# Kernel tuning notes

Hardware: AMD Instinct MI355X
Metric: run time of the kernel (lower is better)

## Reference

```python
import jax, jax.numpy as jnp
import numpy as np

B, N, F, T = 16, 1024, 32, 12
K, FC, FT, TS, D = 3, 64, 64, 1, 16
THETA_THR = 0.6
LN_EPS = 1e-5


def setup_inputs() -> dict:
    key = jax.random.key(0)
    ks = jax.random.split(key, 20)
    r = lambda i, shape, s=0.1: jax.random.normal(ks[i], shape, dtype=jnp.float32) * s
    return dict(
        x=jax.random.normal(ks[0], (B, N, F, T), dtype=jnp.float32),
        node_embeddings=r(1, (N, D), 1.0),
        W1=r(2, (T,)), W2=r(3, (F, T)), W3=r(4, (F,)),
        bs=r(5, (1, N, N)), Vs=r(6, (N, N)),
        U1=r(7, (N,)), U2=r(8, (F, N)), U3=r(9, (F,)),
        be=r(10, (1, T, T)), Ve=r(11, (T, T)),
        Theta=r(12, (K, F, FC)),
        tc_v=r(13, (FT, FC, 1, 3)), tc_g=jnp.ones((FT,), jnp.float32), tc_b=r(14, (FT,)),
        rc_w=r(15, (FT, F, 1, 1)), rc_b=r(16, (FT,)),
        ln_w=jnp.ones((FT,), jnp.float32), ln_b=jnp.zeros((FT,), jnp.float32),
    )


def _forward(x, node_embeddings, W1, W2, W3, bs, Vs, U1, U2, U3, be, Ve,
             Theta, tc_v, tc_g, tc_b, rc_w, rc_b, ln_w, ln_b):
    b, n, f, t = x.shape
    k_order = Theta.shape[0]

    # --- temporal attention: E (B,T,T) ---
    lhs = jnp.einsum('bnft,n->btf', x, U1) @ U2                # (B,T,N)
    rhs = jnp.einsum('f,bnft->bnt', U3, x)                     # (B,N,T)
    prod = jnp.einsum('btn,bnu->btu', lhs, rhs)                # (B,T,T)
    E = jnp.einsum('ts,bsu->btu', Ve, jax.nn.sigmoid(prod + be))
    E = jax.nn.softmax(E, axis=1)

    # x_TAt = reshape(B, N*F, T) @ E  (equivalent einsum over t)
    x_TAt = jnp.einsum('bnft,btu->bnfu', x, E)                 # (B,N,F,T)

    # --- sparse spatial attention on x_TAt: (B,N,N) ---
    l2 = jnp.einsum('bnft,t->bnf', x_TAt, W1) @ W2             # (B,N,T)
    r2 = jnp.einsum('f,bnft->btn', W3, x_TAt)                  # (B,T,N)
    prod2 = jnp.einsum('bnt,btm->bnm', l2, r2)                 # (B,N,N)
    S = jnp.einsum('nm,bmk->bnk', Vs, jax.nn.sigmoid(prod2 + bs))
    Sn = jax.nn.softmax(S, axis=1)
    thr = jnp.mean(Sn) / THETA_THR
    spat = jnp.where(Sn < thr, jnp.zeros_like(Sn), Sn)         # Sparse_S_normalized

    # --- K-order adaptive graph conv with attention mask ---
    sup = jax.nn.softmax(jax.nn.relu(node_embeddings @ node_embeddings.T), axis=1)
    polys = [jnp.eye(n, dtype=x.dtype), sup]
    for k in range(2, k_order):
        polys.append(2.0 * sup @ polys[-1] - polys[-2])
    out = jnp.zeros((b, t, n, Theta.shape[2]), x.dtype)
    for k in range(k_order):
        A = polys[k][None] * spat                              # (B,N,N)
        h = jnp.einsum('bnm,bnft->btmf', A, x)                 # A^T @ x per timestep
        out = out + jnp.einsum('btmf,fo->btmo', h, Theta[k])
    gcn = jax.nn.relu(out)                                     # (B,T,N,FC)

    # --- time conv (weight-normed 1x3) + residual 1x1 conv ---
    vnorm = jnp.sqrt(jnp.sum(tc_v * tc_v, axis=(1, 2, 3), keepdims=True))
    w = tc_g[:, None, None, None] * tc_v / vnorm
    inp = gcn.transpose(0, 3, 2, 1)                            # (B,FC,N,T)
    tco = jax.lax.conv_general_dilated(
        inp, w, (1, TS), ((0, 0), (1, 1)),
        dimension_numbers=('NCHW', 'OIHW', 'NCHW')) + tc_b[None, :, None, None]
    res = jax.lax.conv_general_dilated(
        x.transpose(0, 2, 1, 3), rc_w, (1, TS), ((0, 0), (0, 0)),
        dimension_numbers=('NCHW', 'OIHW', 'NCHW')) + rc_b[None, :, None, None]

    # --- layernorm over channel dim ---
    y = (res + tco).transpose(0, 3, 2, 1)                      # (B,T,N,FT)
    mu = jnp.mean(y, axis=-1, keepdims=True)
    var = jnp.var(y, axis=-1, keepdims=True)
    y = (y - mu) / jnp.sqrt(var + LN_EPS) * ln_w + ln_b
    x_res = y.transpose(0, 2, 3, 1)                            # (B,N,FT,T)
    return x_res, spat


def reference(x, node_embeddings, W1, W2, W3, bs, Vs, U1, U2, U3, be, Ve,
              Theta, tc_v, tc_g, tc_b, rc_w, rc_b, ln_w, ln_b):
    return _forward(x, node_embeddings, W1, W2, W3, bs, Vs, U1, U2, U3, be, Ve,
                    Theta, tc_v, tc_g, tc_b, rc_w, rc_b, ln_w, ln_b)
```

## Files before the change

### kernel.cpp

```cpp
#include <hip/hip_runtime.h>
#include <math.h>

#define NB 16
#define NN 1024
#define NF 32
#define NT 12
#define NFC 64
#define NFT 64

typedef __attribute__((ext_vector_type(8))) short bf16x8;
typedef __attribute__((ext_vector_type(4))) float f32x4;

__device__ inline unsigned short cvt_bf(float f) {
    unsigned int u = __float_as_uint(f);
    u += 0x7fff + ((u >> 16) & 1);
    return (unsigned short)(u >> 16);
}
__device__ inline void gll16(const short* g, short* l) {
    __builtin_amdgcn_global_load_lds((const __attribute__((address_space(1))) void*)g,
                                     (__attribute__((address_space(3))) void*)l, 16, 0, 0);
}

__global__ __launch_bounds__(384) void k_pre(const float* __restrict__ x,
                                             const float* __restrict__ U1,
                                             const float* __restrict__ U3,
                                             const float* __restrict__ W3,
                                             float* __restrict__ lhs_pre,
                                             float* __restrict__ rhs,
                                             float* __restrict__ rr3)
{
    __shared__ float xs[8 * 384];
    int b = blockIdx.x, ch = blockIdx.y, tid = threadIdx.x;
    float acc = 0.f;
    for (int c8 = 0; c8 < 8; c8++) {
        int n0 = ch * 64 + c8 * 8;
        size_t r0 = (size_t)b * NN + n0;
        __syncthreads();
        for (int i = 0; i < 8; i++) xs[i * 384 + tid] = x[(r0 + i) * 384 + tid];
        __syncthreads();
        for (int i = 0; i < 8; i++) acc += xs[i * 384 + tid] * U1[n0 + i];
        if (tid < 192) {
            int half = tid / 96;
            int r = tid - half * 96;
            int i = r / 12, t = r - i * 12;
            const float* wv = half ? W3 : U3;
            float s = 0.f;
            for (int f = 0; f < 32; f++) s += wv[f] * xs[i * 384 + f * 12 + t];
            float* outp = half ? rr3 : rhs;
            outp[(r0 + i) * 12 + t] = s;
        }
    }
    int f = tid / 12, t = tid - f * 12;
    atomicAdd(&lhs_pre[b * 384 + t * 32 + f], acc);
}

__global__ __launch_bounds__(256) void k_lhs(const float* __restrict__ lhs_pre,
                                             const float* __restrict__ U2,
                                             float* __restrict__ lhs)
{
    int bt = blockIdx.x;
    int tid = threadIdx.x;
    __shared__ float lp[32];
    if (tid < 32) lp[tid] = lhs_pre[bt * 32 + tid];
    __syncthreads();
    for (int q = 0; q < 4; q++) {
        int n = q * 256 + tid;
        float a = 0.f;
        for (int f = 0; f < 32; f++) a += lp[f] * U2[f * NN + n];
        lhs[(size_t)bt * NN + n] = a;
    }
}

__global__ __launch_bounds__(64) void k_prod(const float* __restrict__ lhs,
                                             const float* __restrict__ rhs,
                                             float* __restrict__ prod)
{
    int blk = blockIdx.x;
    int b = blk / 144, r = blk - b * 144;
    int s = r / 12, u = r - s * 12;
    int tid = threadIdx.x;
    float p = 0.f;
    for (int n = tid; n < NN; n += 64)
        p += lhs[((size_t)b * 12 + s) * NN + n] * rhs[((size_t)b * NN + n) * 12 + u];
    for (int o = 32; o > 0; o >>= 1) p += __shfl_xor(p, o);
    if (tid == 0) prod[blk] = p;
}

__global__ __launch_bounds__(192) void k_E(const float* __restrict__ prod,
                                           const float* __restrict__ be,
                                           const float* __restrict__ Ve,
                                           const float* __restrict__ W1,
                                           float* __restrict__ E,
                                           float* __restrict__ EW1)
{
    int b = blockIdx.x, tid = threadIdx.x;
    __shared__ float ssig[144], sE[144], mx[12], sm[12];
    if (tid < 144) ssig[tid] = 1.f / (1.f + expf(-(prod[b * 144 + tid] + be[tid])));
    __syncthreads();
    if (tid < 144) {
        int t = tid / 12, u = tid - t * 12;
        float a = 0.f;
        for (int s2 = 0; s2 < 12; s2++) a += Ve[t * 12 + s2] * ssig[s2 * 12 + u];
        sE[tid] = a;
    }
    __syncthreads();
    if (tid < 12) {
        float m = -1e30f;
        for (int t = 0; t < 12; t++) m = fmaxf(m, sE[t * 12 + tid]);
        float s = 0.f;
        for (int t = 0; t < 12; t++) s += expf(sE[t * 12 + tid] - m);
        mx[tid] = m; sm[tid] = s;
    }
    __syncthreads();
    float val = 0.f;
    if (tid < 144) {
        int u = tid % 12;
        val = expf(sE[tid] - mx[u]) / sm[u];
        E[b * 144 + tid] = val;
    }
    __syncthreads();
    if (tid < 144) sE[tid] = val;
    __syncthreads();
    if (tid < 12) {
        float a = 0.f;
        for (int u = 0; u < 12; u++) a += sE[tid * 12 + u] * W1[u];
        EW1[b * 12 + tid] = a;
    }
}

__global__ __launch_bounds__(384) void k_l2r2x(const float* __restrict__ x,
                                               const float* __restrict__ rr3,
                                               const float* __restrict__ E,
                                               const float* __restrict__ EW1,
                                               const float* __restrict__ W2,
                                               float* __restrict__ l2,
                                               float* __restrict__ r2)
{
    __shared__ float xs[8 * 384];
    __shared__ float Es[144], ew[12], rrs[96], lp[8][32];
    int b = blockIdx.y, tid = threadIdx.x;
    int n0 = blockIdx.x * 8;
    size_t r0 = (size_t)b * NN + n0;
    if (tid < 144) Es[tid] = E[b * 144 + tid];
    if (tid < 12) ew[tid] = EW1[b * 12 + tid];
    if (tid < 96) rrs[tid] = rr3[(r0 + tid / 12) * 12 + (tid % 12)];
    for (int i = 0; i < 8; i++) xs[i * 384 + tid] = x[(r0 + i) * 384 + tid];
    __syncthreads();
    if (tid < 256) {
        int i = tid >> 5, f = tid & 31;
        float a = 0.f;
#pragma unroll
        for (int t = 0; t < 12; t++) a += xs[i * 384 + f * 12 + t] * ew[t];
        lp[i][f] = a;
    }
    __syncthreads();
    if (tid < 96) {
        int i = tid / 12, u = tid - i * 12;
        float a = 0.f;
        for (int f = 0; f < 32; f++) a += lp[i][f] * W2[f * 12 + u];
        l2[(r0 + i) * 12 + u] = a;
        float rv = 0.f;
#pragma unroll
        for (int t = 0; t < 12; t++) rv += rrs[i * 12 + t] * Es[t * 12 + u];
        r2[((size_t)b * 12 + u) * NN + n0 + i] = rv;
    }
}

__global__ __launch_bounds__(256) void k_Ptile(const float* __restrict__ l2,
                                               const float* __restrict__ r2,
                                               const float* __restrict__ bsin,
                                               unsigned short* __restrict__ Pt)
{
    __shared__ float l2s[64][13];
    __shared__ float r2s[12][64];
    __shared__ float bsS[64][65];
    int k0 = blockIdx.x * 64, m0 = blockIdx.y * 64, b = blockIdx.z;
    int tid = threadIdx.x;
    for (int i = tid; i < 768; i += 256) {
        int r = i / 12, t = i - r * 12;
        l2s[r][t] = l2[((size_t)b * NN + m0 + r) * 12 + t];
    }
    for (int i = tid; i < 768; i += 256) {
        int t = i >> 6, k = i & 63;
        r2s[t][k] = r2[((size_t)b * 12 + t) * NN + k0 + k];
    }
    for (int i = tid; i < 4096; i += 256) {
        int r = i >> 6, c = i & 63;
        bsS[r][c] = bsin[(size_t)(m0 + r) * NN + k0 + c];
    }
    __syncthreads();
    int m = tid & 63, kg = tid >> 6;
    float lv[12];
#pragma unroll
    for (int t = 0; t < 12; t++) lv[t] = l2s[m][t];
#pragma unroll
    for (int s = 0; s < 16; s++) {
        int kl = kg * 16 + s;
        float p = bsS[m][kl];
#pragma unroll
        for (int t = 0; t < 12; t++) p += lv[t] * r2s[t][kl];
        float sg = 1.f / (1.f + expf(-p));
        Pt[((size_t)b * NN + k0 + kl) * NN + m0 + m] = cvt_bf(sg);
    }
}

__global__ __launch_bounds__(256) void k_cvt(const float* __restrict__ s,
                                             unsigned short* __restrict__ d)
{
    size_t i = ((size_t)blockIdx.x * 256 + threadIdx.x) * 4;
    float4 v = *(const float4*)(s + i);
    unsigned int p0 = (unsigned int)cvt_bf(v.x) | ((unsigned int)cvt_bf(v.y) << 16);
    unsigned int p1 = (unsigned int)cvt_bf(v.z) | ((unsigned int)cvt_bf(v.w) << 16);
    *(unsigned int*)(d + i) = p0;
    *(unsigned int*)(d + i + 2) = p1;
}

__global__ __launch_bounds__(256) void k_tb16(const unsigned short* __restrict__ s,
                                              unsigned short* __restrict__ d)
{
    __shared__ unsigned short tl[64][65];
    int r0 = blockIdx.y * 64, c0 = blockIdx.x * 64;
    int tid = threadIdx.x;
    int c = tid & 63, rr = tid >> 6;
    for (int i = 0; i < 16; i++)
        tl[rr + i * 4][c] = s[(size_t)(r0 + rr + i * 4) * NN + c0 + c];
    __syncthreads();
    for (int i = 0; i < 16; i++)
        d[(size_t)(c0 + rr + i * 4) * NN + r0 + c] = tl[c][rr + i * 4];
}

template<int MODE>
__global__ __launch_bounds__(256) void mgemm(const short* __restrict__ A,
                                             const short* __restrict__ B,
                                             void* __restrict__ Cv,
                                             int Kd, int kchunk,
                                             int ldA, int ldB, int ldC,
                                             long sA, long sB, long sC,
                                             float* __restrict__ colsum)
{
    int bz = blockIdx.z;
    const short* Ab = A + (size_t)bz * sA;
    const short* Bb = B + (size_t)bz * sB;
    int i0 = blockIdx.y * 128, j0 = blockIdx.x * 128;
    __shared__ short sm[16384];
    int tid = threadIdx.x;
    int ln = tid & 63, wv = tid >> 6;
    int wm = (wv >> 1) * 64, wn = (wv & 1) * 64;
    int fr = ln & 15, fk = ln >> 4;
    f32x4 acc[4][4];
#pragma unroll
    for (int a = 0; a < 4; a++)
#pragma unroll
        for (int b2 = 0; b2 < 4; b2++) acc[a][b2] = (f32x4)(0.f);

    int k_lo = 0, k_hi = Kd;
    if constexpr (MODE == 3) { k_lo = bz * kchunk; k_hi = k_lo + kchunk; }

    for (int k0 = k_lo; k0 < k_hi; k0 += 64) {
#pragma unroll
        for (int q = 0; q < 4; q++) {
            int e = q * 2048 + tid * 8;
            const short* src = Ab + (size_t)(i0 + (e >> 6)) * ldA + k0 + (e & 63);
            gll16(src, sm + e);
        }
#pragma unroll
        for (int q = 0; q < 4; q++) {
            int e = q * 2048 + tid * 8;
            const short* src = Bb + (size_t)(j0 + (e >> 6)) * ldB + k0 + (e & 63);
            gll16(src, sm + 8192 + e);
        }
        __syncthreads();
#pragma unroll
        for (int ks = 0; ks < 2; ks++) {
            bf16x8 av[4], bv[4];
#pragma unroll
            for (int mi = 0; mi < 4; mi++)
                av[mi] = *(const bf16x8*)(sm + (wm + mi * 16 + fr) * 64 + ks * 32 + fk * 8);
#pragma unroll
            for (int nj = 0; nj < 4; nj++)
                bv[nj] = *(const bf16x8*)(sm + 8192 + (wn + nj * 16 + fr) * 64 + ks * 32 + fk * 8);
#pragma unroll
            for (int mi = 0; mi < 4; mi++)
#pragma unroll
                for (int nj = 0; nj < 4; nj++)
                    acc[mi][nj] = __builtin_amdgcn_mfma_f32_16x16x32_bf16(av[mi], bv[nj], acc[mi][nj], 0, 0, 0);
        }
        __syncthreads();
    }
    if constexpr (MODE == 2) {
        float* Cb = (float*)Cv + (size_t)bz * sC;
#pragma unroll
        for (int nj = 0; nj < 4; nj++) {
            float cs = 0.f;
            int col = j0 + wn + nj * 16 + fr;
#pragma unroll
            for (int mi = 0; mi < 4; mi++) {
                int row = i0 + wm + mi * 16 + fk * 4;
#pragma unroll
                for (int r = 0; r < 4; r++) {
                    float e = expf(acc[mi][nj][r]);
                    Cb[(size_t)(row + r) * ldC + col] = e;
                    cs += e;
                }
            }
            cs += __shfl_xor(cs, 16);
            cs += __shfl_xor(cs, 32);
            if (ln < 16) atomicAdd(&colsum[(size_t)bz * NN + col], cs);
        }
    } else if constexpr (MODE == 3) {
        float* Cb = (float*)Cv;
#pragma unroll
        for (int mi = 0; mi < 4; mi++)
#pragma unroll
            for (int nj = 0; nj < 4; nj++) {
                int row = i0 + wm + mi * 16 + fk * 4;
                int col = j0 + wn + nj * 16 + fr;
#pragma unroll
                for (int r = 0; r < 4; r++)
                    atomicAdd(&Cb[(size_t)(row + r) * ldC + col], acc[mi][nj][r]);
            }
    }
}

__global__ __launch_bounds__(256) void mgemm_h2(const short* __restrict__ A1,
                                                const short* __restrict__ A2,
                                                const short* __restrict__ B,
                                                unsigned short* __restrict__ C1,
                                                unsigned short* __restrict__ C2)
{
    int b = blockIdx.z;
    const short* A1b = A1 + (size_t)b * NN * NN;
    const short* A2b = A2 + (size_t)b * NN * NN;
    const short* Bb  = B  + (size_t)b * 384 * NN;
    int i0 = blockIdx.y * 128, j0 = blockIdx.x * 128;
    __shared__ short sm[24576];
    int tid = threadIdx.x;
    int ln = tid & 63, wv = tid >> 6;
    int wm = (wv >> 1) * 64, wn = (wv & 1) * 64;
    int fr = ln & 15, fk = ln >> 4;
    f32x4 acc1[4][4], acc2[4][4];
#pragma unroll
    for (int a = 0; a < 4; a++)
#pragma unroll
        for (int c = 0; c < 4; c++) { acc1[a][c] = (f32x4)(0.f); acc2[a][c] = (f32x4)(0.f); }

    for (int k0 = 0; k0 < NN; k0 += 64) {
#pragma unroll
        for (int q = 0; q < 4; q++) {
            int e = q * 2048 + tid * 8;
            gll16(A1b + (size_t)(i0 + (e >> 6)) * NN + k0 + (e & 63), sm + e);
        }
#pragma unroll
        for (int q = 0; q < 4; q++) {
            int e = q * 2048 + tid * 8;
            gll16(A2b + (size_t)(i0 + (e >> 6)) * NN + k0 + (e & 63), sm + 8192 + e);
        }
#pragma unroll
        for (int q = 0; q < 4; q++) {
            int e = q * 2048 + tid * 8;
            gll16(Bb + (size_t)(j0 + (e >> 6)) * NN + k0 + (e & 63), sm + 16384 + e);
        }
        __syncthreads();
#pragma unroll
        for (int ks = 0; ks < 2; ks++) {
            bf16x8 a1v[4], a2v[4], bv[4];
#pragma unroll
            for (int mi = 0; mi < 4; mi++) {
                int off = (wm + mi * 16 + fr) * 64 + ks * 32 + fk * 8;
                a1v[mi] = *(const bf16x8*)(sm + off);
                a2v[mi] = *(const bf16x8*)(sm + 8192 + off);
            }
#pragma unroll
            for (int nj = 0; nj < 4; nj++)
                bv[nj] = *(const bf16x8*)(sm + 16384 + (wn + nj * 16 + fr) * 64 + ks * 32 + fk * 8);
#pragma unroll
            for (int mi = 0; mi < 4; mi++)
#pragma unroll
                for (int nj = 0; nj < 4; nj++) {
                    acc1[mi][nj] = __builtin_amdgcn_mfma_f32_16x16x32_bf16(a1v[mi], bv[nj], acc1[mi][nj], 0, 0, 0);
                    acc2[mi][nj] = __builtin_amdgcn_mfma_f32_16x16x32_bf16(a2v[mi], bv[nj], acc2[mi][nj], 0, 0, 0);
                }
        }
        __syncthreads();
    }
#pragma unroll
    for (int mi = 0; mi < 4; mi++)
#pragma unroll
        for (int nj = 0; nj < 4; nj++) {
            int row = i0 + wm + mi * 16 + fk * 4;
            int col = j0 + wn + nj * 16 + fr;
#pragma unroll
            for (int r = 0; r < 4; r++) {
                size_t o = ((size_t)b * NN + row + r) * 384 + col;
                C1[o] = cvt_bf(acc1[mi][nj][r]);
                C2[o] = cvt_bf(acc2[mi][nj][r]);
            }
        }
}

__global__ __launch_bounds__(256) void k_normprep2(float* __restrict__ spat,
                                                   const float* __restrict__ colsum,
                                                   const float* __restrict__ sup,
                                                   const float* __restrict__ supsq,
                                                   unsigned short* __restrict__ At1,
                                                   unsigned short* __restrict__ At2,
                                                   float* __restrict__ sdiag)
{
    __shared__ unsigned short t1[64][66];
    __shared__ unsigned short t2[64][66];
    int b = blockIdx.z;
    int n0 = blockIdx.y * 64, m0 = blockIdx.x * 64;
    int tid = threadIdx.x;
    int c = tid & 63, r0 = tid >> 6;
    const float thr = (1.0f / 1024.0f) / 0.6f;
    float inv = 1.f / colsum[(size_t)b * NN + m0 + c];
    float* sp = spat + (size_t)b * NN * NN;
    for (int i = 0; i < 16; i++) {
        int r = r0 + i * 4;
        size_t idx = (size_t)(n0 + r) * NN + m0 + c;
        float v = sp[idx] * inv;
        v = (v < thr) ? 0.f : v;
        sp[idx] = v;
        if (n0 + r == m0 + c) sdiag[(size_t)b * NN + n0 + r] = v;
        t1[r][c] = cvt_bf(sup[(size_t)(n0 + r) * NN + m0 + c] * v);
        float p2 = 2.f * supsq[(size_t)(n0 + r) * NN + m0 + c]
                 - (((n0 + r) == (m0 + c)) ? 1.f : 0.f);
        t2[r][c] = cvt_bf(p2 * v);
    }
    __syncthreads();
    int c2 = tid & 31, r4 = tid >> 5;
    size_t ob = ((size_t)b * NN + m0) * NN + n0;
    for (int i = 0; i < 8; i++) {
        int rr = r4 + i * 8;
        unsigned int v1 = (unsigned int)t1[2 * c2][rr] | ((unsigned int)t1[2 * c2 + 1][rr] << 16);
        unsigned int v2 = (unsigned int)t2[2 * c2][rr] | ((unsigned int)t2[2 * c2 + 1][rr] << 16);
        *(unsigned int*)(At1 + ob + (size_t)rr * NN + 2 * c2) = v1;
        *(unsigned int*)(At2 + ob + (size_t)rr * NN + 2 * c2) = v2;
    }
}

__global__ __launch_bounds__(256) void k_sup(const float* __restrict__ emb,
                                             float* __restrict__ sup,
                                             unsigned short* __restrict__ supB)
{
    int n = blockIdx.x, tid = threadIdx.x;
    __shared__ float en[16];
    if (tid < 16) en[tid] = emb[n * 16 + tid];
    __syncthreads();
    float v[4];
#pragma unroll
    for (int q = 0; q < 4; q++) {
        int m = q * 256 + tid;
        float d = 0.f;
#pragma unroll
        for (int dd = 0; dd < 16; dd++) d += en[dd] * emb[m * 16 + dd];
        v[q] = fmaxf(d, 0.f);
    }
    float mx = fmaxf(fmaxf(v[0], v[1]), fmaxf(v[2], v[3]));
    for (int o = 32; o > 0; o >>= 1) mx = fmaxf(mx, __shfl_xor(mx, o));
    __shared__ float red[4];
    if ((tid & 63) == 0) red[tid >> 6] = mx;
    __syncthreads();
    mx = fmaxf(fmaxf(red[0], red[1]), fmaxf(red[2], red[3]));
    float e[4];
    float s = 0.f;
#pragma unroll
    for (int q = 0; q < 4; q++) { e[q] = expf(v[q] - mx); s += e[q]; }
    for (int o = 32; o > 0; o >>= 1) s += __shfl_xor(s, o);
    __shared__ float red2[4];
    if ((tid & 63) == 0) red2[tid >> 6] = s;
    __syncthreads();
    s = red2[0] + red2[1] + red2[2] + red2[3];
    float inv = 1.f / s;
#pragma unroll
    for (int q = 0; q < 4; q++) {
        float val = e[q] * inv;
        sup[(size_t)n * NN + q * 256 + tid] = val;
        supB[(size_t)n * NN + q * 256 + tid] = cvt_bf(val);
    }
}

__global__ __launch_bounds__(256) void k_xt(const float* __restrict__ x,
                                            unsigned short* __restrict__ Xt)
{
    __shared__ float tl[64][65];
    int b = blockIdx.z;
    int n0 = blockIdx.y * 64, j0 = blockIdx.x * 64;
    int tid = threadIdx.x;
    int c = tid & 63, r0 = tid >> 6;
    for (int i = 0; i < 16; i++) {
        int r = r0 + i * 4;
        tl[r][c] = x[((size_t)b * NN + n0 + r) * 384 + j0 + c];
    }
    __syncthreads();
    int c2 = tid & 31, r4 = tid >> 5;
    unsigned short* ob = Xt + ((size_t)b * 384 + j0) * NN + n0;
    for (int i = 0; i < 8; i++) {
        int jj = r4 + i * 8;
        unsigned int v0 = cvt_bf(tl[2 * c2][jj]);
        unsigned int v1 = cvt_bf(tl[2 * c2 + 1][jj]);
        *(unsigned int*)(ob + (size_t)jj * NN + 2 * c2) = v0 | (v1 << 16);
    }
}

__global__ __launch_bounds__(192) void k_wnorm(const float* __restrict__ tcv,
                                               const float* __restrict__ tcg,
                                               unsigned short* __restrict__ Wr)
{
    int o = blockIdx.x, tid = threadIdx.x;
    float t = tcv[o * 192 + tid];
    float p = t * t;
    for (int off = 32; off > 0; off >>= 1) p += __shfl_xor(p, off);
    __shared__ float wsr[3];
    if ((tid & 63) == 0) wsr[tid >> 6] = p;
    __syncthreads();
    float sum = wsr[0] + wsr[1] + wsr[2];
    int c = tid / 3, dt = tid - c * 3;
    Wr[o * 192 + dt * 64 + c] = cvt_bf(t * (tcg[o] / sqrtf(sum)));
}

__global__ __launch_bounds__(256) void k_prepw(const float* __restrict__ Theta,
                                               const float* __restrict__ rcw,
                                               unsigned short* __restrict__ Th,
                                               unsigned short* __restrict__ Rc)
{
    int tid = threadIdx.x;
    for (int i = tid; i < 6144; i += 256) {
        int o = i / 96, rem = i - o * 96;
        int kind = rem >> 5, f = rem & 31;
        Th[i] = cvt_bf(Theta[kind * 2048 + f * 64 + o]);
    }
    for (int i = tid; i < 2048; i += 256) Rc[i] = cvt_bf(rcw[i]);
}

__global__ __launch_bounds__(256) void k_tail(const float* __restrict__ x,
                                              const unsigned short* __restrict__ h1,
                                              const unsigned short* __restrict__ h2,
                                              const float* __restrict__ sdiag,
                                              const unsigned short* __restrict__ Th,
                                              const unsigned short* __restrict__ Wr,
                                              const unsigned short* __restrict__ Rc,
                                              const float* __restrict__ tcb,
                                              const float* __restrict__ rcb,
                                              const float* __restrict__ lnw,
                                              const float* __restrict__ lnb,
                                              float* __restrict__ out)
{
    int b = blockIdx.y;
    int node0 = blockIdx.x * 4;
    int tid = threadIdx.x;
    int ln = tid & 63, wv = tid >> 6;
    int fr = ln & 15, fk = ln >> 4;

    __shared__ union {
        struct { unsigned short xt[1920], h1t[1920], h2t[1920], gcn[4032]; } a;
        float Y[48 * 65];
    } u;
    __shared__ float sdp[48];
    __shared__ float lnwS[64], lnbS[64], tbS[64];
    __shared__ float muS[48], rsS[48];

    size_t rowb = ((size_t)b * NN + node0) * 384;
    for (int i = tid; i < 1536; i += 256) {
        int node = i / 384, j = i - node * 384;
        int f = j / 12, t = j - f * 12;
        int la = node * 480 + t * 40 + f;
        u.a.xt[la]  = cvt_bf(x[rowb + i]);
        u.a.h1t[la] = h1[rowb + i];
        u.a.h2t[la] = h2[rowb + i];
    }
    for (int i = tid; i < 576; i += 256) {
        int node = i / 144, r = i - node * 144;
        int rr = (r < 72) ? 0 : 13;
        u.a.gcn[node * 1008 + rr * 72 + (r % 72)] = 0;
    }
    if (tid < 48) sdp[tid] = sdiag[(size_t)b * NN + node0 + tid / 12];
    if (tid < 64) { lnwS[tid] = lnw[tid]; lnbS[tid] = lnb[tid]; tbS[tid] = tcb[tid] + rcb[tid]; }

    int ocol = wv * 16 + fr;
    bf16x8 bTh[3], bWr[6], bRc;
#pragma unroll
    for (int kb = 0; kb < 3; kb++)
        bTh[kb] = *(const bf16x8*)((const short*)Th + (size_t)ocol * 96 + kb * 32 + fk * 8);
#pragma unroll
    for (int kb = 0; kb < 6; kb++)
        bWr[kb] = *(const bf16x8*)((const short*)Wr + (size_t)ocol * 192 + kb * 32 + fk * 8);
    bRc = *(const bf16x8*)((const short*)Rc + (size_t)ocol * 32 + fk * 8);

    int na[3], ta[3];
#pragma unroll
    for (int rb = 0; rb < 3; rb++) {
        int p = rb * 16 + fr;
        na[rb] = p / 12; ta[rb] = p - na[rb] * 12;
    }
    __syncthreads();

    f32x4 acc[3];
#pragma unroll
    for (int rb = 0; rb < 3; rb++) {
        int ax = na[rb] * 480 + ta[rb] * 40 + fk * 8;
        bf16x8 avx = *(const bf16x8*)(u.a.xt + ax);
        f32x4 z = (f32x4)(0.f);
        acc[rb] = __builtin_amdgcn_mfma_f32_16x16x32_bf16(avx, bTh[0], z, 0, 0, 0);
#pragma unroll
        for (int r = 0; r < 4; r++) acc[rb][r] *= sdp[rb * 16 + fk * 4 + r];
        bf16x8 av1 = *(const bf16x8*)(u.a.h1t + ax);
        acc[rb] = __builtin_amdgcn_mfma_f32_16x16x32_bf16(av1, bTh[1], acc[rb], 0, 0, 0);
        bf16x8 av2 = *(const bf16x8*)(u.a.h2t + ax);
        acc[rb] = __builtin_amdgcn_mfma_f32_16x16x32_bf16(av2, bTh[2], acc[rb], 0, 0, 0);
    }
#pragma unroll
    for (int rb = 0; rb < 3; rb++) {
#pragma unroll
        for (int r = 0; r < 4; r++) {
            int pc = rb * 16 + fk * 4 + r;
            int nc = pc / 12, tc2 = pc - nc * 12;
            u.a.gcn[nc * 1008 + (tc2 + 1) * 72 + wv * 16 + fr] = cvt_bf(fmaxf(acc[rb][r], 0.f));
        }
    }
    __syncthreads();
#pragma unroll
    for (int rb = 0; rb < 3; rb++) {
        f32x4 a2 = (f32x4)(0.f);
#pragma unroll
        for (int kb = 0; kb < 6; kb++) {
            int dt = kb >> 1, c0 = (kb & 1) * 32;
            bf16x8 ag = *(const bf16x8*)(u.a.gcn + na[rb] * 1008 + (ta[rb] + dt) * 72 + c0 + fk * 8);
            a2 = __builtin_amdgcn_mfma_f32_16x16x32_bf16(ag, bWr[kb], a2, 0, 0, 0);
        }
        int ax = na[rb] * 480 + ta[rb] * 40 + fk * 8;
        bf16x8 avx = *(const bf16x8*)(u.a.xt + ax);
        acc[rb] = __builtin_amdgcn_mfma_f32_16x16x32_bf16(avx, bRc, a2, 0, 0, 0);
    }
    __syncthreads();
    float tb = tbS[ocol];
#pragma unroll
    for (int rb = 0; rb < 3; rb++)
#pragma unroll
        for (int r = 0; r < 4; r++)
            u.Y[(rb * 16 + fk * 4 + r) * 65 + ocol] = acc[rb][r] + tb;
    __syncthreads();
    if (tid < 48) {
        float s = 0.f, s2 = 0.f;
        for (int o = 0; o < 64; o++) {
            float v = u.Y[tid * 65 + o];
            s += v; s2 += v * v;
        }
        float mm = s * (1.f / 64.f);
        float var = s2 * (1.f / 64.f) - mm * mm;
        muS[tid] = mm; rsS[tid] = rsqrtf(var + 1e-5f);
    }
    __syncthreads();
    float* ob = out + rowb * 2;
    for (int i = tid; i < 3072; i += 256) {
        int node = i / 768, rr = i - node * 768;
        int o = rr / 12, t = rr - o * 12;
        int p = node * 12 + t;
        ob[i] = (u.Y[p * 65 + o] - muS[p]) * rsS[p] * lnwS[o] + lnbS[o];
    }
}

extern "C" void kernel_launch(void* const* d_in, const int* in_sizes, int n_in,
                              void* d_out, int out_size, void* d_ws, size_t ws_size,
                              hipStream_t stream)
{
    const float* x    = (const float*)d_in[0];
    const float* emb  = (const float*)d_in[1];
    const float* W1   = (const float*)d_in[2];
    const float* W2   = (const float*)d_in[3];
    const float* W3   = (const float*)d_in[4];
    const float* bs   = (const float*)d_in[5];
    const float* Vs   = (const float*)d_in[6];
    const float* U1   = (const float*)d_in[7];
    const float* U2   = (const float*)d_in[8];
    const float* U3   = (const float*)d_in[9];
    const float* be   = (const float*)d_in[10];
    const float* Ve   = (const float*)d_in[11];
    const float* Theta= (const float*)d_in[12];
    const float* tcv  = (const float*)d_in[13];
    const float* tcg  = (const float*)d_in[14];
    const float* tcb  = (const float*)d_in[15];
    const float* rcw  = (const float*)d_in[16];
    const float* rcb  = (const float*)d_in[17];
    const float* lnw  = (const float*)d_in[18];
    const float* lnb  = (const float*)d_in[19];

    float* xres = (float*)d_out;
    float* spat = xres + (size_t)NB * NN * NFT * NT;

    char* base = (char*)d_ws;
    unsigned short* Pt   = (unsigned short*)(base + 0);
    unsigned short* supB = (unsigned short*)(base + 0);
    unsigned short* supT = (unsigned short*)(base + 2097152);
    unsigned short* At1  = (unsigned short*)(base + 0);
    unsigned short* At2  = (unsigned short*)xres;
    unsigned short* Xt  = (unsigned short*)(base + 33554432);
    unsigned short* h1  = (unsigned short*)(base + 46137344);
    unsigned short* h2  = (unsigned short*)(base + 58720256);
    unsigned short* Vsb = (unsigned short*)(base + 71303168);
    float* colsum  = (float*)(base + 73400320);
    float* sdiag   = (float*)(base + 73465856);
    float* sup     = (float*)(base + 77594624);
    float* supsq   = (float*)(base + 81788928);
    float* lhs_pre = (float*)(base + 85983232);
    float* lhs     = (float*)(base + 86007808);
    float* rhs     = (float*)(base + 86794240);
    float* rr3     = (float*)(base + 87580672);
    float* prod    = (float*)(base + 88367104);
    float* E       = (float*)(base + 88376320);
    float* EW1     = (float*)(base + 88385536);
    float* l2      = (float*)(base + 88386560);
    float* r2      = (float*)(base + 89172992);
    unsigned short* Wr = (unsigned short*)(base + 89959424);
    unsigned short* Th = (unsigned short*)(base + 89984000);
    unsigned short* Rc = (unsigned short*)(base + 89996288);

    hipMemsetAsync(lhs_pre, 0, 6144 * sizeof(float), stream);
    hipMemsetAsync(supsq, 0, (size_t)NN * NN * sizeof(float), stream);

    k_pre<<<dim3(16, 16), 384, 0, stream>>>(x, U1, U3, W3, lhs_pre, rhs, rr3);
    k_lhs<<<192, 256, 0, stream>>>(lhs_pre, U2, lhs);
    k_prod<<<2304, 64, 0, stream>>>(lhs, rhs, prod);
    k_E<<<16, 192, 0, stream>>>(prod, be, Ve, W1, E, EW1);
    k_l2r2x<<<dim3(128, 16), 384, 0, stream>>>(x, rr3, E, EW1, W2, l2, r2);
    k_Ptile<<<dim3(16, 16, 16), 256, 0, stream>>>(l2, r2, bs, Pt);
    k_cvt<<<1024, 256, 0, stream>>>(Vs, Vsb);
    hipMemsetAsync(colsum, 0, (size_t)NB * NN * sizeof(float), stream);
    mgemm<2><<<dim3(8, 8, 16), 256, 0, stream>>>((const short*)Vsb, (const short*)Pt,
        (void*)spat, NN, 0, NN, NN, NN, 0L, (long)NN * NN, (long)NN * NN, colsum);
    k_sup<<<1024, 256, 0, stream>>>(emb, sup, supB);
    k_tb16<<<dim3(16, 16), 256, 0, stream>>>(supB, supT);
    mgemm<3><<<dim3(8, 8, 4), 256, 0, stream>>>((const short*)supB, (const short*)supT,
        (void*)supsq, NN, 256, NN, NN, NN, 0L, 0L, 0L, nullptr);
    k_normprep2<<<dim3(16, 16, 16), 256, 0, stream>>>(spat, colsum, sup, supsq, At1, At2, sdiag);
    k_xt<<<dim3(6, 16, 16), 256, 0, stream>>>(x, Xt);
    mgemm_h2<<<dim3(3, 8, 16), 256, 0, stream>>>((const short*)At1, (const short*)At2,
        (const short*)Xt, h1, h2);
    k_wnorm<<<64, 192, 0, stream>>>(tcv, tcg, Wr);
    k_prepw<<<1, 256, 0, stream>>>(Theta, rcw, Th, Rc);
    k_tail<<<dim3(256, 16), 256, 0, stream>>>(x, h1, h2, sdiag, Th, Wr, Rc,
                                              tcb, rcb, lnw, lnb, xres);
}
```

Measured before the change: 353.5 us.

## Split dual-output h GEMM into two XCD-mapped GEMMs and stage x as bf16

The fused two-A GEMM (h1 and h2 sharing the Xt operand) becomes two launches of a single-output GEMM. Each launch has half the accumulators and a smaller LDS footprint, and blocks are mapped so that each XCD handles two batches. In exchange, Xt is loaded twice. k_pre now also writes a bf16 row copy of x; k_l2r2x reads that copy instead of fp32 x, which halves its load bytes but lowers the precision of l2. The transpose kernel k_xt now reads the bf16 copy and is launched earlier in the sequence.

```diff
diff --git a/kernel.cpp b/kernel.cpp
--- a/kernel.cpp
+++ b/kernel.cpp
@@ -16,6 +16,9 @@
     u += 0x7fff + ((u >> 16) & 1);
     return (unsigned short)(u >> 16);
 }
+__device__ inline float bf2f(unsigned short u) {
+    return __uint_as_float(((unsigned int)u) << 16);
+}
 __device__ inline void gll16(const short* g, short* l) {
     __builtin_amdgcn_global_load_lds((const __attribute__((address_space(1))) void*)g,
                                      (__attribute__((address_space(3))) void*)l, 16, 0, 0);
@@ -27,7 +30,8 @@
                                              const float* __restrict__ W3,
                                              float* __restrict__ lhs_pre,
                                              float* __restrict__ rhs,
-                                             float* __restrict__ rr3)
+                                             float* __restrict__ rr3,
+                                             unsigned short* __restrict__ Xrow)
 {
     __shared__ float xs[8 * 384];
     int b = blockIdx.x, ch = blockIdx.y, tid = threadIdx.x;
@@ -38,7 +42,11 @@
         __syncthreads();
         for (int i = 0; i < 8; i++) xs[i * 384 + tid] = x[(r0 + i) * 384 + tid];
         __syncthreads();
-        for (int i = 0; i < 8; i++) acc += xs[i * 384 + tid] * U1[n0 + i];
+        for (int i = 0; i < 8; i++) {
+            float v = xs[i * 384 + tid];
+            acc += v * U1[n0 + i];
+            Xrow[(r0 + i) * 384 + tid] = cvt_bf(v);
+        }
         if (tid < 192) {
             int half = tid / 96;
             int r = tid - half * 96;
@@ -128,7 +136,7 @@
     }
 }
 
-__global__ __launch_bounds__(384) void k_l2r2x(const float* __restrict__ x,
+__global__ __launch_bounds__(384) void k_l2r2x(const unsigned short* __restrict__ Xrow,
                                                const float* __restrict__ rr3,
                                                const float* __restrict__ E,
                                                const float* __restrict__ EW1,
@@ -144,7 +152,7 @@
     if (tid < 144) Es[tid] = E[b * 144 + tid];
     if (tid < 12) ew[tid] = EW1[b * 12 + tid];
     if (tid < 96) rrs[tid] = rr3[(r0 + tid / 12) * 12 + (tid % 12)];
-    for (int i = 0; i < 8; i++) xs[i * 384 + tid] = x[(r0 + i) * 384 + tid];
+    for (int i = 0; i < 8; i++) xs[i * 384 + tid] = bf2f(Xrow[(r0 + i) * 384 + tid]);
     __syncthreads();
     if (tid < 256) {
         int i = tid >> 5, f = tid & 31;
@@ -163,6 +171,28 @@
 #pragma unroll
         for (int t = 0; t < 12; t++) rv += rrs[i * 12 + t] * Es[t * 12 + u];
         r2[((size_t)b * 12 + u) * NN + n0 + i] = rv;
+    }
+}
+
+__global__ __launch_bounds__(256) void k_xt(const unsigned short* __restrict__ Xrow,
+                                            unsigned short* __restrict__ Xt)
+{
+    __shared__ unsigned short tl[64][66];
+    int b = blockIdx.z;
+    int n0 = blockIdx.y * 64, j0 = blockIdx.x * 64;
+    int tid = threadIdx.x;
+    int c = tid & 63, r0 = tid >> 6;
+    for (int i = 0; i < 16; i++) {
+        int r = r0 + i * 4;
+        tl[r][c] = Xrow[((size_t)b * NN + n0 + r) * 384 + j0 + c];
+    }
+    __syncthreads();
+    int c2 = tid & 31, r4 = tid >> 5;
+    unsigned short* ob = Xt + ((size_t)b * 384 + j0) * NN + n0;
+    for (int i = 0; i < 8; i++) {
+        int jr = r4 + i * 8;
+        unsigned int v0 = (unsigned int)tl[2 * c2][jr] | ((unsigned int)tl[2 * c2 + 1][jr] << 16);
+        *(unsigned int*)(ob + (size_t)jr * NN + 2 * c2) = v0;
     }
 }
 
@@ -322,64 +352,54 @@
     }
 }
 
-__global__ __launch_bounds__(256) void mgemm_h2(const short* __restrict__ A1,
-                                                const short* __restrict__ A2,
-                                                const short* __restrict__ B,
-                                                unsigned short* __restrict__ C1,
-                                                unsigned short* __restrict__ C2)
-{
-    int b = blockIdx.z;
-    const short* A1b = A1 + (size_t)b * NN * NN;
-    const short* A2b = A2 + (size_t)b * NN * NN;
-    const short* Bb  = B  + (size_t)b * 384 * NN;
-    int i0 = blockIdx.y * 128, j0 = blockIdx.x * 128;
-    __shared__ short sm[24576];
+__global__ __launch_bounds__(256) void mgemm_h(const short* __restrict__ A,
+                                               const short* __restrict__ B,
+                                               unsigned short* __restrict__ C)
+{
+    int id = blockIdx.x;
+    int xcd = id & 7, jj = id >> 3;
+    int b = (xcd << 1) | (jj / 24);
+    int r = jj % 24;
+    int i0 = (r / 3) * 128, j0 = (r % 3) * 128;
+    const short* Ab = A + (size_t)b * NN * NN;
+    const short* Bb = B + (size_t)b * 384 * NN;
+    __shared__ short sm[16384];
     int tid = threadIdx.x;
     int ln = tid & 63, wv = tid >> 6;
     int wm = (wv >> 1) * 64, wn = (wv & 1) * 64;
     int fr = ln & 15, fk = ln >> 4;
-    f32x4 acc1[4][4], acc2[4][4];
+    f32x4 acc[4][4];
 #pragma unroll
     for (int a = 0; a < 4; a++)
 #pragma unroll
-        for (int c = 0; c < 4; c++) { acc1[a][c] = (f32x4)(0.f); acc2[a][c] = (f32x4)(0.f); }
+        for (int b2 = 0; b2 < 4; b2++) acc[a][b2] = (f32x4)(0.f);
 
     for (int k0 = 0; k0 < NN; k0 += 64) {
 #pragma unroll
         for (int q = 0; q < 4; q++) {
             int e = q * 2048 + tid * 8;
-            gll16(A1b + (size_t)(i0 + (e >> 6)) * NN + k0 + (e & 63), sm + e);
+            gll16(Ab + (size_t)(i0 + (e >> 6)) * NN + k0 + (e & 63), sm + e);
         }
 #pragma unroll
         for (int q = 0; q < 4; q++) {
             int e = q * 2048 + tid * 8;
-            gll16(A2b + (size_t)(i0 + (e >> 6)) * NN + k0 + (e & 63), sm + 8192 + e);
-        }
-#pragma unroll
-        for (int q = 0; q < 4; q++) {
-            int e = q * 2048 + tid * 8;
-            gll16(Bb + (size_t)(j0 + (e >> 6)) * NN + k0 + (e & 63), sm + 16384 + e);
+            gll16(Bb + (size_t)(j0 + (e >> 6)) * NN + k0 + (e & 63), sm + 8192 + e);
         }
         __syncthreads();
 #pragma unroll
         for (int ks = 0; ks < 2; ks++) {
-            bf16x8 a1v[4], a2v[4], bv[4];
-#pragma unroll
-            for (int mi = 0; mi < 4; mi++) {
-                int off = (wm + mi * 16 + fr) * 64 + ks * 32 + fk * 8;
-                a1v[mi] = *(const bf16x8*)(sm + off);
-                a2v[mi] = *(const bf16x8*)(sm + 8192 + off);
-            }
+            bf16x8 av[4], bv[4];
+#pragma unroll
+            for (int mi = 0; mi < 4; mi++)
+                av[mi] = *(const bf16x8*)(sm + (wm + mi * 16 + fr) * 64 + ks * 32 + fk * 8);
 #pragma unroll
             for (int nj = 0; nj < 4; nj++)
-                bv[nj] = *(const bf16x8*)(sm + 16384 + (wn + nj * 16 + fr) * 64 + ks * 32 + fk * 8);
+                bv[nj] = *(const bf16x8*)(sm + 8192 + (wn + nj * 16 + fr) * 64 + ks * 32 + fk * 8);
 #pragma unroll
             for (int mi = 0; mi < 4; mi++)
 #pragma unroll
-                for (int nj = 0; nj < 4; nj++) {
-                    acc1[mi][nj] = __builtin_amdgcn_mfma_f32_16x16x32_bf16(a1v[mi], bv[nj], acc1[mi][nj], 0, 0, 0);
-                    acc2[mi][nj] = __builtin_amdgcn_mfma_f32_16x16x32_bf16(a2v[mi], bv[nj], acc2[mi][nj], 0, 0, 0);
-                }
+                for (int nj = 0; nj < 4; nj++)
+                    acc[mi][nj] = __builtin_amdgcn_mfma_f32_16x16x32_bf16(av[mi], bv[nj], acc[mi][nj], 0, 0, 0);
         }
         __syncthreads();
     }
@@ -390,11 +410,8 @@
             int row = i0 + wm + mi * 16 + fk * 4;
             int col = j0 + wn + nj * 16 + fr;
 #pragma unroll
-            for (int r = 0; r < 4; r++) {
-                size_t o = ((size_t)b * NN + row + r) * 384 + col;
-                C1[o] = cvt_bf(acc1[mi][nj][r]);
-                C2[o] = cvt_bf(acc2[mi][nj][r]);
-            }
+            for (int r2 = 0; r2 < 4; r2++)
+                C[((size_t)b * NN + row + r2) * 384 + col] = cvt_bf(acc[mi][nj][r2]);
         }
 }
 
@@ -477,29 +494,6 @@
         float val = e[q] * inv;
         sup[(size_t)n * NN + q * 256 + tid] = val;
         supB[(size_t)n * NN + q * 256 + tid] = cvt_bf(val);
-    }
-}
-
-__global__ __launch_bounds__(256) void k_xt(const float* __restrict__ x,
-                                            unsigned short* __restrict__ Xt)
-{
-    __shared__ float tl[64][65];
-    int b = blockIdx.z;
-    int n0 = blockIdx.y * 64, j0 = blockIdx.x * 64;
-    int tid = threadIdx.x;
-    int c = tid & 63, r0 = tid >> 6;
-    for (int i = 0; i < 16; i++) {
-        int r = r0 + i * 4;
-        tl[r][c] = x[((size_t)b * NN + n0 + r) * 384 + j0 + c];
-    }
-    __syncthreads();
-    int c2 = tid & 31, r4 = tid >> 5;
-    unsigned short* ob = Xt + ((size_t)b * 384 + j0) * NN + n0;
-    for (int i = 0; i < 8; i++) {
-        int jj = r4 + i * 8;
-        unsigned int v0 = cvt_bf(tl[2 * c2][jj]);
-        unsigned int v1 = cvt_bf(tl[2 * c2 + 1][jj]);
-        *(unsigned int*)(ob + (size_t)jj * NN + 2 * c2) = v0 | (v1 << 16);
     }
 }
 
@@ -689,6 +683,7 @@
     float* spat = xres + (size_t)NB * NN * NFT * NT;
 
     char* base = (char*)d_ws;
+    unsigned short* Xrow = (unsigned short*)(base + 0);
     unsigned short* Pt   = (unsigned short*)(base + 0);
     unsigned short* supB = (unsigned short*)(base + 0);
     unsigned short* supT = (unsigned short*)(base + 2097152);
@@ -718,11 +713,12 @@
     hipMemsetAsync(lhs_pre, 0, 6144 * sizeof(float), stream);
     hipMemsetAsync(supsq, 0, (size_t)NN * NN * sizeof(float), stream);
 
-    k_pre<<<dim3(16, 16), 384, 0, stream>>>(x, U1, U3, W3, lhs_pre, rhs, rr3);
+    k_pre<<<dim3(16, 16), 384, 0, stream>>>(x, U1, U3, W3, lhs_pre, rhs, rr3, Xrow);
     k_lhs<<<192, 256, 0, stream>>>(lhs_pre, U2, lhs);
     k_prod<<<2304, 64, 0, stream>>>(lhs, rhs, prod);
     k_E<<<16, 192, 0, stream>>>(prod, be, Ve, W1, E, EW1);
-    k_l2r2x<<<dim3(128, 16), 384, 0, stream>>>(x, rr3, E, EW1, W2, l2, r2);
+    k_l2r2x<<<dim3(128, 16), 384, 0, stream>>>(Xrow, rr3, E, EW1, W2, l2, r2);
+    k_xt<<<dim3(6, 16, 16), 256, 0, stream>>>(Xrow, Xt);
     k_Ptile<<<dim3(16, 16, 16), 256, 0, stream>>>(l2, r2, bs, Pt);
     k_cvt<<<1024, 256, 0, stream>>>(Vs, Vsb);
     hipMemsetAsync(colsum, 0, (size_t)NB * NN * sizeof(float), stream);
@@ -733,9 +729,8 @@
     mgemm<3><<<dim3(8, 8, 4), 256, 0, stream>>>((const short*)supB, (const short*)supT,
         (void*)supsq, NN, 256, NN, NN, NN, 0L, 0L, 0L, nullptr);
     k_normprep2<<<dim3(16, 16, 16), 256, 0, stream>>>(spat, colsum, sup, supsq, At1, At2, sdiag);
-    k_xt<<<dim3(6, 16, 16), 256, 0, stream>>>(x, Xt);
-    mgemm_h2<<<dim3(3, 8, 16), 256, 0, stream>>>((const short*)At1, (const short*)At2,
-        (const short*)Xt, h1, h2);
+    mgemm_h<<<384, 256, 0, stream>>>((const short*)At1, (const short*)Xt, h1);
+    mgemm_h<<<384, 256, 0, stream>>>((const short*)At2, (const short*)Xt, h2);
     k_wnorm<<<64, 192, 0, stream>>>(tcv, tcg, Wr);
     k_prepw<<<1, 256, 0, stream>>>(Theta, rcw, Th, Rc);
     k_tail<<<dim3(256, 16), 256, 0, stream>>>(x, h1, h2, sdiag, Th, Wr, Rc,
```

Measured after the change: 337.3 us. -4.6%, faster.
